# Optimization experiments

Measured on AMD Instinct MI355X. Metric: run time of the kernel, lower is better.

The kernel has to match this reference:

```python
import jax, jax.numpy as jnp
import numpy as np

B, N, E = 128, 50000, 1600000


def setup_inputs() -> dict:
    key = jax.random.key(0)
    k1, k2, k3, k4, k5 = jax.random.split(key, 5)
    x = jax.random.normal(k1, (B, N), dtype=jnp.float32)
    h = jax.random.normal(k2, (N,), dtype=jnp.float32)
    J = jax.random.normal(k3, (E,), dtype=jnp.float32)
    edge_idx_i = jax.random.randint(k4, (E,), 0, N, dtype=jnp.int64) if jax.config.jax_enable_x64 else jax.random.randint(k4, (E,), 0, N, dtype=jnp.int32)
    edge_idx_j = jax.random.randint(k5, (E,), 0, N, dtype=jnp.int32)
    return {"x": x, "h": h, "J": J, "edge_idx_i": edge_idx_i, "edge_idx_j": edge_idx_j}


def reference(x, h, J, edge_idx_i, edge_idx_j):
    # Hamiltonian: H(x) = x @ h + (x[:, ei] * x[:, ej]) @ J  -> shape (B,)
    interactions = x[:, edge_idx_i] * x[:, edge_idx_j]  # (B, E)
    return x @ h + interactions @ J
```

## Files before the change

### kernel.cpp

```cpp
#include <hip/hip_runtime.h>
#include <hip/hip_bf16.h>
#include <hip/hip_fp16.h>

#define BDIM    128
#define NGROUPS 4
#define GCOLS   32
#define ROWB    (GCOLS * 2)
#define EBLK    2048
#define RANKS   (EBLK / NGROUPS)
#define CHUNK   256
#define S1BLK   (NGROUPS * 8)
#define HBLK2   8
#define RPS     (RANKS / 8)

__global__ __launch_bounds__(256) void transpose_h_kernel(
    const float* __restrict__ x, const float* __restrict__ h,
    __half* __restrict__ xTh, float* __restrict__ hp, int N) {
  __shared__ float tile[64][BDIM + 1];
  __shared__ float sh[64];
  __shared__ float red2[2][BDIM];
  const int tid = threadIdx.x;
  const int n0  = blockIdx.x * 64;

  const int tn  = tid & 63;
  const int tb0 = tid >> 6;
  const int n   = n0 + tn;
  if (n < N) {
    for (int b = tb0; b < BDIM; b += 4) tile[tn][b] = x[(size_t)b * N + n];
  } else {
    for (int b = tb0; b < BDIM; b += 4) tile[tn][b] = 0.f;
  }
  if (tid < 64) sh[tid] = (n0 + tid < N) ? h[n0 + tid] : 0.f;
  __syncthreads();

  const int hb   = tid & 127;
  const int half = tid >> 7;
  float hacc = 0.f;
#pragma unroll
  for (int m = 0; m < 32; ++m) {
    const int nl = half * 32 + m;
    hacc += tile[nl][hb] * sh[nl];
  }
  red2[half][hb] = hacc;

  const int c2 = tid & 15;
  const int g2 = (tid >> 4) & 3;
  const int k  = tid >> 6;
  for (int it = 0; it < 16; ++it) {
    const int nl = it * 4 + k;
    if (n0 + nl < N) {
      const float a = tile[nl][g2 * GCOLS + 2 * c2];
      const float b = tile[nl][g2 * GCOLS + 2 * c2 + 1];
      __half2* dst = (__half2*)(xTh + ((size_t)g2 * N + (n0 + nl)) * GCOLS + 2 * c2);
      *dst = __floats2half2_rn(a, b);
    }
  }
  __syncthreads();
  if (tid < BDIM) hp[(size_t)blockIdx.x * BDIM + tid] = red2[0][tid] + red2[1][tid];
}

__global__ __launch_bounds__(256) void edge_kernel(
    const __half* __restrict__ xTh, const float* __restrict__ J,
    const int* __restrict__ ei, const int* __restrict__ ej,
    float* __restrict__ partials, int E, int N, int edges_per_rank) {
  const int tid  = threadIdx.x;
  const int g    = (blockIdx.x & 7) >> 1;
  const int rank = (blockIdx.x >> 3) * 2 + (blockIdx.x & 1);
  const char* xgl = (const char*)(xTh + (size_t)g * N * GCOLS) + (tid & 3) * 16;

  const int wave = tid >> 6;
  const int lane = tid & 63;
  const int k    = lane >> 2;
  const int q    = lane & 3;

  const int start = rank * edges_per_rank;
  const int end   = min(start + edges_per_rank, E);

  __shared__ int2  sij[CHUNK];
  __shared__ float sJ[CHUNK];

  int ri = 0, rj = 0;
  float rJ = 0.f;
  {
    const int e = start + tid;
    if (e < end) { ri = ei[e]; rj = ej[e]; rJ = J[e]; }
  }

  float acc[8] = {0.f, 0.f, 0.f, 0.f, 0.f, 0.f, 0.f, 0.f};

  for (int base = start; base < end; base += CHUNK) {
    sij[tid] = make_int2(ri, rj);
    sJ[tid]  = rJ;
    __syncthreads();

    {
      const int e = base + CHUNK + tid;
      ri = 0; rj = 0; rJ = 0.f;
      if (e < end) { ri = ei[e]; rj = ej[e]; rJ = J[e]; }
    }

    const int lbase = wave * 64 + k;
#pragma unroll
    for (int u = 0; u < 4; ++u) {
      const int   l  = lbase + u * 16;
      const int2  ij = sij[l];
      const float Jv = sJ[l];
      const int4 vi = *(const int4*)(xgl + (unsigned)ij.x * ROWB);
      const int4 vj = *(const int4*)(xgl + (unsigned)ij.y * ROWB);
      const int wi[4] = {vi.x, vi.y, vi.z, vi.w};
      const int wj[4] = {vj.x, vj.y, vj.z, vj.w};
#pragma unroll
      for (int w = 0; w < 4; ++w) {
        const __half2 hi = __builtin_bit_cast(__half2, wi[w]);
        const __half2 hj = __builtin_bit_cast(__half2, wj[w]);
        const __half2 p  = __hmul2(hi, hj);
        acc[2 * w]     += __low2float(p)  * Jv;
        acc[2 * w + 1] += __high2float(p) * Jv;
      }
    }
    __syncthreads();
  }

#pragma unroll
  for (int off = 4; off < 64; off <<= 1)
#pragma unroll
    for (int w = 0; w < 8; ++w) acc[w] += __shfl_xor(acc[w], off);

  __shared__ float red[4][GCOLS];
  if (lane < 4)
#pragma unroll
    for (int w = 0; w < 8; ++w) red[wave][q * 8 + w] = acc[w];
  __syncthreads();
  if (tid < GCOLS) {
    const float s = red[0][tid] + red[1][tid] + red[2][tid] + red[3][tid];
    partials[((size_t)g * RANKS + rank) * GCOLS + tid] = s;
  }
}

__global__ __launch_bounds__(256) void reduce1_kernel(
    const float* __restrict__ P, const float* __restrict__ hp,
    float* __restrict__ P2, float* __restrict__ hp2, int hrows) {
  __shared__ float red[8][GCOLS];
  __shared__ float redh[2][BDIM];
  if (blockIdx.x < S1BLK) {
    const int g  = blockIdx.x >> 3;
    const int s  = blockIdx.x & 7;
    const int rl = threadIdx.x >> 5;
    const int c  = threadIdx.x & 31;
    float acc = 0.f;
    for (int rr = rl; rr < RPS; rr += 8)
      acc += P[((size_t)g * RANKS + s * RPS + rr) * GCOLS + c];
    red[rl][c] = acc;
    __syncthreads();
    if (threadIdx.x < GCOLS) {
      float sum = 0.f;
      for (int r = 0; r < 8; ++r) sum += red[r][threadIdx.x];
      P2[(size_t)blockIdx.x * GCOLS + threadIdx.x] = sum;
    }
  } else {
    const int s  = blockIdx.x - S1BLK;
    const int b  = threadIdx.x & 127;
    const int rg = threadIdx.x >> 7;
    float acc = 0.f;
    for (int r = s + 8 * rg; r < hrows; r += 16)
      acc += hp[(size_t)r * BDIM + b];
    redh[rg][b] = acc;
    __syncthreads();
    if (threadIdx.x < BDIM)
      hp2[(size_t)s * BDIM + threadIdx.x] = redh[0][threadIdx.x] + redh[1][threadIdx.x];
  }
}

__global__ __launch_bounds__(128) void reduce2_kernel(
    const float* __restrict__ P2, const float* __restrict__ hp2,
    float* __restrict__ out) {
  const int b = threadIdx.x;
  const int g = b >> 5;
  const int c = b & 31;
  float acc = 0.f;
  for (int s = 0; s < 8; ++s) acc += hp2[(size_t)s * BDIM + b];
  for (int s = 0; s < 8; ++s) acc += P2[(size_t)(g * 8 + s) * GCOLS + c];
  out[b] = acc;
}

extern "C" void kernel_launch(void* const* d_in, const int* in_sizes, int n_in,
                              void* d_out, int out_size, void* d_ws, size_t ws_size,
                              hipStream_t stream) {
  const float* x  = (const float*)d_in[0];
  const float* h  = (const float*)d_in[1];
  const float* J  = (const float*)d_in[2];
  const int*   ei = (const int*)d_in[3];
  const int*   ej = (const int*)d_in[4];
  float* out = (float*)d_out;

  const int N = in_sizes[1];
  const int E = in_sizes[2];

  const int tblocks = (N + 63) / 64;

  __half* xTh = (__half*)d_ws;
  float* P   = (float*)(xTh + (size_t)NGROUPS * N * GCOLS);
  float* P2  = P   + (size_t)EBLK * GCOLS;
  float* hp  = P2  + (size_t)S1BLK * GCOLS;
  float* hp2 = hp  + (size_t)tblocks * BDIM;

  transpose_h_kernel<<<tblocks, 256, 0, stream>>>(x, h, xTh, hp, N);

  const int epr = (E + RANKS - 1) / RANKS;
  edge_kernel<<<EBLK, 256, 0, stream>>>(xTh, J, ei, ej, P, E, N, epr);

  reduce1_kernel<<<S1BLK + HBLK2, 256, 0, stream>>>(P, hp, P2, hp2, tblocks);

  reduce2_kernel<<<1, BDIM, 0, stream>>>(P2, hp2, out);
}
```

Baseline: 91.91 us.

## Drop LDS staging in edge kernel; give each wave its own edge range

The edge kernel no longer stages edge indices and weights through shared memory with block-wide barriers. Each wave now owns a contiguous edge range and loads indices directly from global memory, processing two edges per lane-group per iteration to get more gathers in flight. Launch bounds now request higher occupancy. In exchange, the index loads are now direct and less coalesced per wave, and the previous cross-chunk prefetch is gone.

New measurement: 95.66 us. 1.04x slower.

```diff
diff --git a/kernel.cpp b/kernel.cpp
--- a/kernel.cpp
+++ b/kernel.cpp
@@ -8,7 +8,7 @@
 #define ROWB    (GCOLS * 2)
 #define EBLK    2048
 #define RANKS   (EBLK / NGROUPS)
-#define CHUNK   256
+#define WPG     (RANKS * 4)
 #define S1BLK   (NGROUPS * 8)
 #define HBLK2   8
 #define RPS     (RANKS / 8)
@@ -59,66 +59,61 @@
   if (tid < BDIM) hp[(size_t)blockIdx.x * BDIM + tid] = red2[0][tid] + red2[1][tid];
 }
 
-__global__ __launch_bounds__(256) void edge_kernel(
+__device__ __forceinline__ void fma8(float* acc, int4 vi, int4 vj, float Jv) {
+  const int wi[4] = {vi.x, vi.y, vi.z, vi.w};
+  const int wj[4] = {vj.x, vj.y, vj.z, vj.w};
+#pragma unroll
+  for (int w = 0; w < 4; ++w) {
+    const __half2 hi = __builtin_bit_cast(__half2, wi[w]);
+    const __half2 hj = __builtin_bit_cast(__half2, wj[w]);
+    const __half2 p  = __hmul2(hi, hj);
+    acc[2 * w]     += __low2float(p)  * Jv;
+    acc[2 * w + 1] += __high2float(p) * Jv;
+  }
+}
+
+__global__ __launch_bounds__(256, 8) void edge_kernel(
     const __half* __restrict__ xTh, const float* __restrict__ J,
     const int* __restrict__ ei, const int* __restrict__ ej,
-    float* __restrict__ partials, int E, int N, int edges_per_rank) {
+    float* __restrict__ partials, int E, int N, int edges_per_wave) {
   const int tid  = threadIdx.x;
   const int g    = (blockIdx.x & 7) >> 1;
   const int rank = (blockIdx.x >> 3) * 2 + (blockIdx.x & 1);
-  const char* xgl = (const char*)(xTh + (size_t)g * N * GCOLS) + (tid & 3) * 16;
-
   const int wave = tid >> 6;
   const int lane = tid & 63;
   const int k    = lane >> 2;
-  const int q    = lane & 3;
-
-  const int start = rank * edges_per_rank;
-  const int end   = min(start + edges_per_rank, E);
-
-  __shared__ int2  sij[CHUNK];
-  __shared__ float sJ[CHUNK];
-
-  int ri = 0, rj = 0;
-  float rJ = 0.f;
-  {
-    const int e = start + tid;
-    if (e < end) { ri = ei[e]; rj = ej[e]; rJ = J[e]; }
-  }
+  const char* xgl = (const char*)xTh + (size_t)g * N * ROWB + (lane & 3) * 16;
+
+  const int ws = (rank * 4 + wave) * edges_per_wave;
+  const int we = min(ws + edges_per_wave, E);
 
   float acc[8] = {0.f, 0.f, 0.f, 0.f, 0.f, 0.f, 0.f, 0.f};
 
-  for (int base = start; base < end; base += CHUNK) {
-    sij[tid] = make_int2(ri, rj);
-    sJ[tid]  = rJ;
-    __syncthreads();
-
-    {
-      const int e = base + CHUNK + tid;
-      ri = 0; rj = 0; rJ = 0.f;
-      if (e < end) { ri = ei[e]; rj = ej[e]; rJ = J[e]; }
-    }
-
-    const int lbase = wave * 64 + k;
-#pragma unroll
-    for (int u = 0; u < 4; ++u) {
-      const int   l  = lbase + u * 16;
-      const int2  ij = sij[l];
-      const float Jv = sJ[l];
-      const int4 vi = *(const int4*)(xgl + (unsigned)ij.x * ROWB);
-      const int4 vj = *(const int4*)(xgl + (unsigned)ij.y * ROWB);
-      const int wi[4] = {vi.x, vi.y, vi.z, vi.w};
-      const int wj[4] = {vj.x, vj.y, vj.z, vj.w};
-#pragma unroll
-      for (int w = 0; w < 4; ++w) {
-        const __half2 hi = __builtin_bit_cast(__half2, wi[w]);
-        const __half2 hj = __builtin_bit_cast(__half2, wj[w]);
-        const __half2 p  = __hmul2(hi, hj);
-        acc[2 * w]     += __low2float(p)  * Jv;
-        acc[2 * w + 1] += __high2float(p) * Jv;
-      }
-    }
-    __syncthreads();
+  int e0 = (ws < E) ? ws : E;
+  for (; e0 + 32 <= we; e0 += 32) {
+    const int eA = e0 + k;
+    const int eB = eA + 16;
+    const int   iA = ei[eA];
+    const int   jA = ej[eA];
+    const float JA = J[eA];
+    const int   iB = ei[eB];
+    const int   jB = ej[eB];
+    const float JB = J[eB];
+    const int4 viA = *(const int4*)(xgl + (unsigned)iA * ROWB);
+    const int4 vjA = *(const int4*)(xgl + (unsigned)jA * ROWB);
+    const int4 viB = *(const int4*)(xgl + (unsigned)iB * ROWB);
+    const int4 vjB = *(const int4*)(xgl + (unsigned)jB * ROWB);
+    fma8(acc, viA, vjA, JA);
+    fma8(acc, viB, vjB, JB);
+  }
+  for (; e0 < we; e0 += 16) {
+    const int e = e0 + k;
+    int i = 0, j = 0;
+    float Jv = 0.f;
+    if (e < we) { i = ei[e]; j = ej[e]; Jv = J[e]; }
+    const int4 vi = *(const int4*)(xgl + (unsigned)i * ROWB);
+    const int4 vj = *(const int4*)(xgl + (unsigned)j * ROWB);
+    fma8(acc, vi, vj, Jv);
   }
 
 #pragma unroll
@@ -129,7 +124,7 @@
   __shared__ float red[4][GCOLS];
   if (lane < 4)
 #pragma unroll
-    for (int w = 0; w < 8; ++w) red[wave][q * 8 + w] = acc[w];
+    for (int w = 0; w < 8; ++w) red[wave][(lane & 3) * 8 + w] = acc[w];
   __syncthreads();
   if (tid < GCOLS) {
     const float s = red[0][tid] + red[1][tid] + red[2][tid] + red[3][tid];
@@ -206,8 +201,8 @@
 
   transpose_h_kernel<<<tblocks, 256, 0, stream>>>(x, h, xTh, hp, N);
 
-  const int epr = (E + RANKS - 1) / RANKS;
-  edge_kernel<<<EBLK, 256, 0, stream>>>(xTh, J, ei, ej, P, E, N, epr);
+  const int epw = (((E + WPG - 1) / WPG) + 31) & ~31;
+  edge_kernel<<<EBLK, 256, 0, stream>>>(xTh, J, ei, ej, P, E, N, epw);
 
   reduce1_kernel<<<S1BLK + HBLK2, 256, 0, stream>>>(P, hp, P2, hp2, tblocks);
 
```

## Widen batch column groups to 64 and fuse half products with fma_mix

Applied to the files above, without the earlier changes.

Splits the batch into two 64-column groups instead of four 32-column groups, so each gathered row is 128 bytes and each edge is processed by 8 lanes, with 2 groups × 1024 ranks. Edge indices and J are packed into one int4 in shared memory, so each edge needs a single LDS read. The half-to-float conversion and FMA are fused through inline v_fma_mix_f32. The aim is to halve redundant index/J traffic and edge passes per group and to cut ALU instructions, at the cost of wider gathers per edge and fewer ranks per group.

Measured after the change: 83.64 us. 9.0% less time.

```diff
diff --git a/kernel.cpp b/kernel.cpp
--- a/kernel.cpp
+++ b/kernel.cpp
@@ -3,8 +3,8 @@
 #include <hip/hip_fp16.h>
 
 #define BDIM    128
-#define NGROUPS 4
-#define GCOLS   32
+#define NGROUPS 2
+#define GCOLS   64
 #define ROWB    (GCOLS * 2)
 #define EBLK    2048
 #define RANKS   (EBLK / NGROUPS)
@@ -43,8 +43,8 @@
   }
   red2[half][hb] = hacc;
 
-  const int c2 = tid & 15;
-  const int g2 = (tid >> 4) & 3;
+  const int c2 = tid & 31;
+  const int g2 = (tid >> 5) & 1;
   const int k  = tid >> 6;
   for (int it = 0; it < 16; ++it) {
     const int nl = it * 4 + k;
@@ -59,25 +59,37 @@
   if (tid < BDIM) hp[(size_t)blockIdx.x * BDIM + tid] = red2[0][tid] + red2[1][tid];
 }
 
+__device__ __forceinline__ void fma8mix(float* acc, int4 vi, int4 vj, float Jv) {
+  const int wi[4] = {vi.x, vi.y, vi.z, vi.w};
+  const int wj[4] = {vj.x, vj.y, vj.z, vj.w};
+#pragma unroll
+  for (int w = 0; w < 4; ++w) {
+    const __half2 hi = __builtin_bit_cast(__half2, wi[w]);
+    const __half2 hj = __builtin_bit_cast(__half2, wj[w]);
+    const int p = __builtin_bit_cast(int, __hmul2(hi, hj));
+    asm("v_fma_mix_f32 %0, %1, %2, %0 op_sel_hi:[1,0,0]"
+        : "+v"(acc[2 * w]) : "v"(p), "v"(Jv));
+    asm("v_fma_mix_f32 %0, %1, %2, %0 op_sel:[1,0,0] op_sel_hi:[1,0,0]"
+        : "+v"(acc[2 * w + 1]) : "v"(p), "v"(Jv));
+  }
+}
+
 __global__ __launch_bounds__(256) void edge_kernel(
     const __half* __restrict__ xTh, const float* __restrict__ J,
     const int* __restrict__ ei, const int* __restrict__ ej,
-    float* __restrict__ partials, int E, int N, int edges_per_rank) {
+    float* __restrict__ P, int E, int N, int epr) {
   const int tid  = threadIdx.x;
-  const int g    = (blockIdx.x & 7) >> 1;
-  const int rank = (blockIdx.x >> 3) * 2 + (blockIdx.x & 1);
-  const char* xgl = (const char*)(xTh + (size_t)g * N * GCOLS) + (tid & 3) * 16;
-
+  const int g    = (blockIdx.x & 7) >> 2;
+  const int rank = (blockIdx.x >> 3) * 4 + (blockIdx.x & 3);
   const int wave = tid >> 6;
   const int lane = tid & 63;
-  const int k    = lane >> 2;
-  const int q    = lane & 3;
-
-  const int start = rank * edges_per_rank;
-  const int end   = min(start + edges_per_rank, E);
-
-  __shared__ int2  sij[CHUNK];
-  __shared__ float sJ[CHUNK];
+  const int k    = lane >> 3;
+  const char* xgl = (const char*)xTh + (size_t)g * N * ROWB + (lane & 7) * 16;
+
+  const int start = rank * epr;
+  const int end   = min(start + epr, E);
+
+  __shared__ int4 se[CHUNK];
 
   int ri = 0, rj = 0;
   float rJ = 0.f;
@@ -89,8 +101,7 @@
   float acc[8] = {0.f, 0.f, 0.f, 0.f, 0.f, 0.f, 0.f, 0.f};
 
   for (int base = start; base < end; base += CHUNK) {
-    sij[tid] = make_int2(ri, rj);
-    sJ[tid]  = rJ;
+    se[tid] = make_int4(ri, rj, __float_as_int(rJ), 0);
     __syncthreads();
 
     {
@@ -101,60 +112,50 @@
 
     const int lbase = wave * 64 + k;
 #pragma unroll
-    for (int u = 0; u < 4; ++u) {
-      const int   l  = lbase + u * 16;
-      const int2  ij = sij[l];
-      const float Jv = sJ[l];
-      const int4 vi = *(const int4*)(xgl + (unsigned)ij.x * ROWB);
-      const int4 vj = *(const int4*)(xgl + (unsigned)ij.y * ROWB);
-      const int wi[4] = {vi.x, vi.y, vi.z, vi.w};
-      const int wj[4] = {vj.x, vj.y, vj.z, vj.w};
-#pragma unroll
-      for (int w = 0; w < 4; ++w) {
-        const __half2 hi = __builtin_bit_cast(__half2, wi[w]);
-        const __half2 hj = __builtin_bit_cast(__half2, wj[w]);
-        const __half2 p  = __hmul2(hi, hj);
-        acc[2 * w]     += __low2float(p)  * Jv;
-        acc[2 * w + 1] += __high2float(p) * Jv;
-      }
-    }
-    __syncthreads();
-  }
-
-#pragma unroll
-  for (int off = 4; off < 64; off <<= 1)
+    for (int u = 0; u < 8; ++u) {
+      const int4  eJ = se[lbase + u * 8];
+      const float Jv = __int_as_float(eJ.z);
+      const int4 vi = *(const int4*)(xgl + (unsigned)eJ.x * ROWB);
+      const int4 vj = *(const int4*)(xgl + (unsigned)eJ.y * ROWB);
+      fma8mix(acc, vi, vj, Jv);
+    }
+    __syncthreads();
+  }
+
+#pragma unroll
+  for (int off = 8; off < 64; off <<= 1)
 #pragma unroll
     for (int w = 0; w < 8; ++w) acc[w] += __shfl_xor(acc[w], off);
 
   __shared__ float red[4][GCOLS];
-  if (lane < 4)
-#pragma unroll
-    for (int w = 0; w < 8; ++w) red[wave][q * 8 + w] = acc[w];
+  if (lane < 8)
+#pragma unroll
+    for (int w = 0; w < 8; ++w) red[wave][lane * 8 + w] = acc[w];
   __syncthreads();
   if (tid < GCOLS) {
     const float s = red[0][tid] + red[1][tid] + red[2][tid] + red[3][tid];
-    partials[((size_t)g * RANKS + rank) * GCOLS + tid] = s;
+    P[((size_t)g * RANKS + rank) * GCOLS + tid] = s;
   }
 }
 
 __global__ __launch_bounds__(256) void reduce1_kernel(
     const float* __restrict__ P, const float* __restrict__ hp,
     float* __restrict__ P2, float* __restrict__ hp2, int hrows) {
-  __shared__ float red[8][GCOLS];
+  __shared__ float red[4][GCOLS];
   __shared__ float redh[2][BDIM];
   if (blockIdx.x < S1BLK) {
     const int g  = blockIdx.x >> 3;
     const int s  = blockIdx.x & 7;
-    const int rl = threadIdx.x >> 5;
-    const int c  = threadIdx.x & 31;
+    const int rl = threadIdx.x >> 6;
+    const int c  = threadIdx.x & 63;
     float acc = 0.f;
-    for (int rr = rl; rr < RPS; rr += 8)
+    for (int rr = rl; rr < RPS; rr += 4)
       acc += P[((size_t)g * RANKS + s * RPS + rr) * GCOLS + c];
     red[rl][c] = acc;
     __syncthreads();
     if (threadIdx.x < GCOLS) {
       float sum = 0.f;
-      for (int r = 0; r < 8; ++r) sum += red[r][threadIdx.x];
+      for (int r = 0; r < 4; ++r) sum += red[r][threadIdx.x];
       P2[(size_t)blockIdx.x * GCOLS + threadIdx.x] = sum;
     }
   } else {
@@ -175,8 +176,8 @@
     const float* __restrict__ P2, const float* __restrict__ hp2,
     float* __restrict__ out) {
   const int b = threadIdx.x;
-  const int g = b >> 5;
-  const int c = b & 31;
+  const int g = b >> 6;
+  const int c = b & 63;
   float acc = 0.f;
   for (int s = 0; s < 8; ++s) acc += hp2[(size_t)s * BDIM + b];
   for (int s = 0; s < 8; ++s) acc += P2[(size_t)(g * 8 + s) * GCOLS + c];
@@ -200,7 +201,7 @@
 
   __half* xTh = (__half*)d_ws;
   float* P   = (float*)(xTh + (size_t)NGROUPS * N * GCOLS);
-  float* P2  = P   + (size_t)EBLK * GCOLS;
+  float* P2  = P   + (size_t)NGROUPS * RANKS * GCOLS;
   float* hp  = P2  + (size_t)S1BLK * GCOLS;
   float* hp2 = hp  + (size_t)tblocks * BDIM;
 
```
